# Kernel optimization log

Hardware: AMD Instinct MI355X
Metric: run time of the kernel (lower is better)

The kernel has to match this reference:

```python
import jax, jax.numpy as jnp
import numpy as np

NT_SIZES = {"paper": 100000, "author": 200000, "subject": 1000}
NT_FEATS = {"paper": 512, "author": 256, "subject": 128}
ET = [("paper", "author"), ("author", "paper"), ("paper", "subject"), ("subject", "paper")]
E_COUNTS = {("paper", "author"): 800000, ("author", "paper"): 800000,
            ("paper", "subject"): 100000, ("subject", "paper"): 100000}
HOP = 5
NHID = 64
NOUT = 16
# edge types sourced at each node type (order follows ET / edge_id mapping)
SRC_IDS = {"paper": [0, 2], "author": [1], "subject": [3]}


def setup_inputs() -> dict:
    key = jax.random.key(0)
    ks = iter(jax.random.split(key, 40))
    inp = {}
    # node features
    inp["x_paper"] = jax.random.normal(next(ks), (NT_SIZES["paper"], NT_FEATS["paper"]), jnp.float32)
    inp["x_author"] = jax.random.normal(next(ks), (NT_SIZES["author"], NT_FEATS["author"]), jnp.float32)
    inp["x_subject"] = jax.random.normal(next(ks), (NT_SIZES["subject"], NT_FEATS["subject"]), jnp.float32)
    # fc1 per node type (torch Linear layout: [out, in]), scaled ~1/sqrt(fan_in)
    for nt in NT_SIZES:
        fin = NT_FEATS[nt]
        inp[f"fc1_{nt}_w"] = jax.random.normal(next(ks), (NHID, fin), jnp.float32) / np.sqrt(fin)
        inp[f"fc1_{nt}_b"] = jnp.zeros((NHID,), jnp.float32)
    # attention vectors per hop per edge type; small scale keeps exp() stable
    inp["attn1_w"] = jax.random.normal(next(ks), (HOP, len(ET), NHID), jnp.float32) * 0.01
    inp["attn2_w"] = jax.random.normal(next(ks), (HOP, len(ET), NHID), jnp.float32) * 0.01
    inp["lw_w"] = jax.random.normal(next(ks), (HOP, len(ET)), jnp.float32)
    inp["fc2_w"] = jax.random.normal(next(ks), (NOUT, NHID), jnp.float32) / np.sqrt(NHID)
    inp["fc2_b"] = jnp.zeros((NOUT,), jnp.float32)
    # edge indices: row 0 = source (in src node-type range), row 1 = target
    for (s_nt, t_nt) in ET:
        E = E_COUNTS[(s_nt, t_nt)]
        s = jax.random.randint(next(ks), (E,), 0, NT_SIZES[s_nt], jnp.int32)
        t = jax.random.randint(next(ks), (E,), 0, NT_SIZES[t_nt], jnp.int32)
        inp[f"ei_{s_nt[0]}{t_nt[0]}"] = jnp.stack([s, t])
    return inp


def reference(x_paper, x_author, x_subject,
              fc1_paper_w, fc1_paper_b, fc1_author_w, fc1_author_b,
              fc1_subject_w, fc1_subject_b,
              attn1_w, attn2_w, lw_w, fc2_w, fc2_b,
              ei_pa, ei_ap, ei_ps, ei_sp):
    x_in = {"paper": x_paper, "author": x_author, "subject": x_subject}
    fc1 = {"paper": (fc1_paper_w, fc1_paper_b),
           "author": (fc1_author_w, fc1_author_b),
           "subject": (fc1_subject_w, fc1_subject_b)}
    edges = {ET[0]: ei_pa, ET[1]: ei_ap, ET[2]: ei_ps, ET[3]: ei_sp}

    # input projection (dropout = identity in eval mode)
    x_dict = {nt: jax.nn.relu(x_in[nt] @ fc1[nt][0].T + fc1[nt][1]) for nt in x_in}
    h_dict = dict(x_dict)

    for i in range(HOP):
        aggr = {nt: [] for nt in x_dict}
        for k, et in enumerate(ET):
            s_nt, t_nt = et
            ei = edges[et]
            s, t = ei[0], ei[1]
            x = x_dict[s_nt]            # [Ns, D]
            h = h_dict[t_nt]            # [Nt, D]
            N = x.shape[0]
            a1 = attn1_w[i, k]          # [D]
            a2 = attn2_w[i, k]          # [D]
            x1 = x @ a1                 # [Ns]
            h1 = h @ a2                 # [Nt]
            w2 = jnp.exp(jax.nn.leaky_relu(x1 + x @ a2, 0.2))            # [Ns] self term
            w1 = jnp.exp(jax.nn.leaky_relu(x1[s] + h1[t], 0.2))          # [E]  edge term
            div = jax.ops.segment_sum(w1, s, num_segments=N) + w2        # [Ns]
            num = jax.ops.segment_sum(w1[:, None] * h[t], s, num_segments=N) + w2[:, None] * x
            aggr[s_nt].append(num / div[:, None])
        for nt in x_dict:
            ids = jnp.array(SRC_IDS[nt])
            w = jax.nn.softmax(lw_w[i, ids])                             # learnable per-edge-type mix
            stacked = jnp.stack(aggr[nt], axis=1)                        # [N, K, D]
            h_dict[nt] = jax.nn.elu(jnp.einsum('nkd,k->nd', stacked, w))
    return h_dict["paper"] @ fc2_w.T + fc2_b
```

## Files before the change

kernel.cpp:

```cpp
#include <hip/hip_runtime.h>
#include <hip/hip_bf16.h>


#define NP 100000
#define NA 200000
#define NSJ 1000
#define EPA 800000
#define EAP 800000
#define EPS 100000
#define ESP 100000
#define ETOT 1800000
#define NS_TOT 401000
#define NT_TOT 401000
#define NSRC 301000
#define NCHUNK 392
#define NSGRP 25063
#define SCAT_SLICE 4096
#define NSLICE ((ETOT + SCAT_SLICE - 1) / SCAT_SLICE)
#define BKT ((ETOT + 7) / 8)

typedef __attribute__((ext_vector_type(8))) short bf16x8;
typedef __attribute__((ext_vector_type(4))) float floatx4;
typedef __attribute__((ext_vector_type(8))) float floatx8;
typedef __hip_bfloat16 bf16;

__device__ __forceinline__ float bf2f(bf16 v) { return __bfloat162float(v); }
__device__ __forceinline__ float us2f(unsigned short u) { return __uint_as_float((unsigned)u << 16); }
__device__ __forceinline__ float eluf(float x) { return x > 0.f ? x : __expf(x) - 1.f; }
__device__ __forceinline__ unsigned short f2bf_bits(float f) {
    unsigned int u = __float_as_uint(f);
    return (unsigned short)((u + 0x7FFFu + ((u >> 16) & 1u)) >> 16);
}

__device__ __forceinline__ bf16x8 load_frag_f32(const void* base, size_t off) {
    const float4* f = (const float4*)((const float*)base + off);
    float4 a = f[0], b = f[1];
    bf16x8 r;
    r[0] = (short)f2bf_bits(a.x); r[1] = (short)f2bf_bits(a.y);
    r[2] = (short)f2bf_bits(a.z); r[3] = (short)f2bf_bits(a.w);
    r[4] = (short)f2bf_bits(b.x); r[5] = (short)f2bf_bits(b.y);
    r[6] = (short)f2bf_bits(b.z); r[7] = (short)f2bf_bits(b.w);
    return r;
}

__device__ __forceinline__ int edge_src(int e, const int* pa, const int* ap,
                                        const int* ps, const int* sp) {
    if (e < EPA)                  return pa[e];
    if (e < EPA + EAP)            return NP + ap[e - EPA];
    if (e < EPA + EAP + EPS)      return NP + NA + ps[e - (EPA + EAP)];
    return NP + NA + NP + sp[e - (EPA + EAP + EPS)];
}
__device__ __forceinline__ int edge_tgt(int e, const int* pa, const int* ap,
                                        const int* ps, const int* sp) {
    if (e < EPA)                  return pa[EPA + e];
    if (e < EPA + EAP)            return ap[EAP + (e - EPA)];
    if (e < EPA + EAP + EPS)      return ps[EPS + (e - (EPA + EAP))];
    return sp[ESP + (e - (EPA + EAP + EPS))];
}

__global__ void detect_dtype(const unsigned int* __restrict__ xraw, int* __restrict__ flag) {
    int t = threadIdx.x;
    int hits = 0;
#pragma unroll
    for (int i = 0; i < 16; ++i) {
        unsigned int w = xraw[t * 16 + i];
        unsigned int lo = w & 0xFFFFu;
        unsigned int e = (lo >> 7) & 0xFFu;
        if (lo == 0u || (e >= 110u && e <= 140u)) hits++;
    }
#pragma unroll
    for (int o = 32; o; o >>= 1) hits += __shfl_xor(hits, o);
    if (t == 0) *flag = (hits > 512) ? 1 : 0;
}

__global__ void conv_all(const void* a1, const void* a2, const void* lw, const void* w2,
                         const void* b2, const void* bp, const void* ba, const void* bs,
                         float* a1c, float* a2c, float* lwc, float* w2c, float* b2c,
                         float* b1p, float* b1a, float* b1s, const int* __restrict__ flagp)
{
    int i = blockIdx.x * blockDim.x + threadIdx.x;
    int isb = *flagp;
    auto cv = [&](const void* s, int j) -> float {
        return isb ? bf2f(((const bf16*)s)[j]) : ((const float*)s)[j];
    };
    if (i < 1280)      a1c[i] = cv(a1, i);
    else if (i < 2560) a2c[i - 1280] = cv(a2, i - 1280);
    else if (i < 2580) lwc[i - 2560] = cv(lw, i - 2560);
    else if (i < 3604) w2c[i - 2580] = cv(w2, i - 2580);
    else if (i < 3620) b2c[i - 3604] = cv(b2, i - 3604);
    else if (i < 3684) b1p[i - 3620] = cv(bp, i - 3620);
    else if (i < 3748) b1a[i - 3684] = cv(ba, i - 3684);
    else if (i < 3812) b1s[i - 3748] = cv(bs, i - 3748);
}

__global__ void pack_attn(const float* __restrict__ a1c, const float* __restrict__ a2c,
                          bf16* __restrict__ apack)
{
    int i = blockIdx.x * blockDim.x + threadIdx.x;
    if (i >= 4096) return;
    int k = i >> 10, rf = i & 1023;
    int row = rf >> 6;
    int f = rf & 63;
    float v = 0.f;
    if (row < 5)       v = a1c[(row * 4 + k) * 64 + f];
    else if (row < 10) v = a2c[((row - 5) * 4 + k) * 64 + f];
    unsigned short hi = f2bf_bits(v);
    float lo = v - us2f(hi);
    unsigned short* up = (unsigned short*)apack;
    up[(size_t)(k * 2) * 1024 + rf]     = hi;
    up[(size_t)(k * 2 + 1) * 1024 + rf] = f2bf_bits(lo);
}

template<int K>
__global__ void fc1_t(const void* __restrict__ X, const void* __restrict__ W,
                      const float* __restrict__ B, int N,
                      bf16* __restrict__ xo, const int* __restrict__ flagp)
{
    constexpr int NK = K / 32;
    int isb = *flagp;
    int lane = threadIdx.x & 63;
    int wv = threadIdx.x >> 6;
    int grp = blockIdx.x * 4 + wv;
    int ngrp = (N + 15) >> 4;
    if (grp >= ngrp) return;
    int m = lane & 15, kq = lane >> 4;
    floatx4 acc[4] = {};
    int arow = grp * 16 + m;
    if (arow >= N) arow = N - 1;
    if (isb) {
        const bf16* Xb = (const bf16*)X + (size_t)arow * K + kq * 8;
        bf16x8 av[NK];
#pragma unroll
        for (int i = 0; i < NK; ++i) av[i] = *(const bf16x8*)(Xb + i * 32);
        const bf16* Wb = (const bf16*)W + (size_t)m * K + kq * 8;
#pragma unroll
        for (int i = 0; i < NK; ++i) {
#pragma unroll
            for (int nb = 0; nb < 4; ++nb) {
                bf16x8 bv = *(const bf16x8*)(Wb + (size_t)(nb * 16) * K + i * 32);
                acc[nb] = __builtin_amdgcn_mfma_f32_16x16x32_bf16(av[i], bv, acc[nb], 0, 0, 0);
            }
        }
    } else {
#pragma unroll 4
        for (int i = 0; i < NK; ++i) {
            int k0 = i * 32 + kq * 8;
            bf16x8 av = load_frag_f32(X, (size_t)arow * K + k0);
#pragma unroll
            for (int nb = 0; nb < 4; ++nb) {
                bf16x8 bv = load_frag_f32(W, (size_t)(nb * 16 + m) * K + k0);
                acc[nb] = __builtin_amdgcn_mfma_f32_16x16x32_bf16(av, bv, acc[nb], 0, 0, 0);
            }
        }
    }
#pragma unroll
    for (int nb = 0; nb < 4; ++nb) {
#pragma unroll
        for (int r = 0; r < 4; ++r) {
            int row = grp * 16 + kq * 4 + r;
            if (row < N) {
                int f = nb * 16 + m;
                float v = acc[nb][r] + B[f];
                xo[(size_t)row * 64 + f] = __float2bfloat16(fmaxf(v, 0.f));
            }
        }
    }
}

__global__ void precompute_xw_mfma(const bf16* __restrict__ xP, const bf16* __restrict__ xA,
                                   const bf16* __restrict__ xS,
                                   const bf16* __restrict__ apack,
                                   float* __restrict__ x1buf, float* __restrict__ w2buf)
{
    int wv = threadIdx.x >> 6;
    int lane = threadIdx.x & 63;
    int grp = blockIdx.x * 4 + wv;
    if (grp >= NSGRP) return;
    int base = grp * 16;
    int k, n0, nmax; const bf16* x;
    if (base < NP)                { k = 0; n0 = base;                  nmax = NP;  x = xP; }
    else if (base < NP + NA)      { k = 1; n0 = base - NP;             nmax = NA;  x = xA; }
    else if (base < NP + NA + NP) { k = 2; n0 = base - (NP + NA);      nmax = NP;  x = xP; }
    else                          { k = 3; n0 = base - (NP + NA + NP); nmax = NSJ; x = xS; }
    int m = lane & 15, kq = lane >> 4;
    int arow = n0 + m;
    if (arow >= nmax) arow = nmax - 1;
    const bf16* bh = apack + (size_t)(k * 2) * 1024;
    const bf16* bl = bh + 1024;
    floatx4 acc = {};
#pragma unroll
    for (int ks = 0; ks < 64; ks += 32) {
        int k0 = ks + kq * 8;
        bf16x8 av  = *(const bf16x8*)(x  + (size_t)arow * 64 + k0);
        bf16x8 bvh = *(const bf16x8*)(bh + m * 64 + k0);
        bf16x8 bvl = *(const bf16x8*)(bl + m * 64 + k0);
        acc = __builtin_amdgcn_mfma_f32_16x16x32_bf16(av, bvh, acc, 0, 0, 0);
        acc = __builtin_amdgcn_mfma_f32_16x16x32_bf16(av, bvl, acc, 0, 0, 0);
    }
#pragma unroll
    for (int r = 0; r < 4; ++r) {
        float v = acc[r];
        float d2 = __shfl(v, lane + 5);
        int node = base + kq * 4 + r;
        if (m < 5 && node < NS_TOT) {
            x1buf[m * NS_TOT + node] = v;
            float z = v + d2;
            w2buf[m * NS_TOT + node] = __expf(z > 0.f ? z : 0.2f * z);
        }
    }
}

__global__ void csr_rank(const int* __restrict__ pa, const int* __restrict__ ap,
                         const int* __restrict__ ps, const int* __restrict__ sp,
                         int* __restrict__ cnt, int* __restrict__ rank)
{
    int e = blockIdx.x * blockDim.x + threadIdx.x;
    if (e >= ETOT) return;
    int g = edge_src(e, pa, ap, ps, sp);
    rank[e] = atomicAdd(&cnt[g], 1);
}

__global__ void scan_reduce(const int* __restrict__ cnt, int* __restrict__ partial)
{
    __shared__ int s[256];
    int base = blockIdx.x * 1024 + threadIdx.x * 4;
    int sum = 0;
#pragma unroll
    for (int r = 0; r < 4; ++r) { int i = base + r; if (i < NS_TOT) sum += cnt[i]; }
    s[threadIdx.x] = sum; __syncthreads();
    for (int o = 128; o; o >>= 1) {
        if (threadIdx.x < o) s[threadIdx.x] += s[threadIdx.x + o];
        __syncthreads();
    }
    if (!threadIdx.x) partial[blockIdx.x] = s[0];
}

__global__ void scan_partials(const int* __restrict__ partial, int* __restrict__ chunkoff)
{
    __shared__ int s[512];
    int t = threadIdx.x;
    int v = (t < NCHUNK) ? partial[t] : 0;
    s[t] = v; __syncthreads();
    for (int o = 1; o < 512; o <<= 1) {
        int add = (t >= o) ? s[t - o] : 0;
        __syncthreads();
        s[t] += add; __syncthreads();
    }
    if (t < NCHUNK) chunkoff[t] = s[t] - v;
}

__global__ void scan_write(const int* __restrict__ cnt, const int* __restrict__ chunkoff,
                           int* __restrict__ off)
{
    __shared__ int s[256];
    int t = threadIdx.x;
    int base = blockIdx.x * 1024 + t * 4;
    int v[4]; int tsum = 0;
#pragma unroll
    for (int r = 0; r < 4; ++r) { int i = base + r; v[r] = (i < NS_TOT) ? cnt[i] : 0; tsum += v[r]; }
    s[t] = tsum; __syncthreads();
    for (int o = 1; o < 256; o <<= 1) {
        int add = (t >= o) ? s[t - o] : 0;
        __syncthreads();
        s[t] += add; __syncthreads();
    }
    int excl = s[t] - tsum + chunkoff[blockIdx.x];
#pragma unroll
    for (int r = 0; r < 4; ++r) {
        int i = base + r;
        if (i < NS_TOT) { off[i] = excl; excl += v[r]; }
    }
}

__global__ void csr_pos(const int* __restrict__ pa, const int* __restrict__ ap,
                        const int* __restrict__ ps, const int* __restrict__ sp,
                        const int* __restrict__ rank, const int* __restrict__ off,
                        int* __restrict__ pos)
{
    int e = blockIdx.x * blockDim.x + threadIdx.x;
    if (e >= ETOT) return;
    int g = edge_src(e, pa, ap, ps, sp);
    pos[e] = off[g] + rank[e];
}

__global__ void csr_scatter(const int* __restrict__ pa, const int* __restrict__ ap,
                            const int* __restrict__ ps, const int* __restrict__ sp,
                            const int* __restrict__ pos, int* __restrict__ col)
{
    int b = blockIdx.x & 7;
    int slice = blockIdx.x >> 3;
    int lo = b * BKT;
    int hi = lo + BKT; if (hi > ETOT) hi = ETOT;
    int ebase = slice * SCAT_SLICE;
    int eend = ebase + SCAT_SLICE; if (eend > ETOT) eend = ETOT;
    for (int e = ebase + threadIdx.x; e < eend; e += 256) {
        int p = pos[e];
        if (p < lo || p >= hi) continue;
        col[p] = edge_tgt(e, pa, ap, ps, sp);
    }
}

__global__ void hop_h1(const bf16* __restrict__ hP, const bf16* __restrict__ hA,
                       const bf16* __restrict__ hS,
                       const float* __restrict__ attn2, int hop, float* __restrict__ h1)
{
    int wave = (blockIdx.x * blockDim.x + threadIdx.x) >> 6;
    int lane = threadIdx.x & 63;
    int q = lane >> 4, fl = lane & 15;
    int wid = wave * 4 + q;
    if (wid >= NT_TOT) return;
    int k, n; const bf16* h;
    if (wid < NA)                 { k = 0; n = wid;               h = hA; }
    else if (wid < NA + NP)       { k = 1; n = wid - NA;          h = hP; }
    else if (wid < NA + NP + NSJ) { k = 2; n = wid - (NA + NP);   h = hS; }
    else                          { k = 3; n = wid - (NA+NP+NSJ); h = hP; }
    ushort4 hv = *(const ushort4*)((const unsigned short*)h + (size_t)n * 64 + fl * 4);
    const float4 a2 = *(const float4*)(attn2 + (hop * 4 + k) * 64 + fl * 4);
    float v = us2f(hv.x) * a2.x + us2f(hv.y) * a2.y + us2f(hv.z) * a2.z + us2f(hv.w) * a2.w;
#pragma unroll
    for (int o = 1; o <= 8; o <<= 1) v += __shfl_xor(v, o);
    if (fl == 0) h1[wid] = v;
}

__device__ __forceinline__ floatx8 agg_et8(int g, int hop, int eo, int fl, floatx8 xv,
    const float* __restrict__ x1buf, const float* __restrict__ w2buf,
    const float* __restrict__ h1, int h1base, const bf16* __restrict__ ht,
    const int* __restrict__ off, const int* __restrict__ deg, const int* __restrict__ col)
{
    float x1v = x1buf[hop * NS_TOT + g];
    floatx8 acc = {};
    float dv = 0.f;
    int e0 = off[g];
    int e1 = e0 + deg[g];
    for (int e = e0 + eo; e < e1; e += 8) {
        int t = col[e];
        float z = x1v + h1[h1base + t];
        float w1 = __expf(z > 0.f ? z : 0.2f * z);
        bf16x8 hv = *(const bf16x8*)(ht + (size_t)t * 64 + fl * 8);
#pragma unroll
        for (int j = 0; j < 8; ++j)
            acc[j] = fmaf(w1, us2f((unsigned short)hv[j]), acc[j]);
        dv += w1;
    }
#pragma unroll
    for (int o = 8; o <= 32; o <<= 1) {
#pragma unroll
        for (int j = 0; j < 8; ++j) acc[j] += __shfl_xor(acc[j], o);
        dv += __shfl_xor(dv, o);
    }
    float w2v = w2buf[hop * NS_TOT + g];
    dv += w2v;
    float inv = 1.f / dv;
    floatx8 r;
#pragma unroll
    for (int j = 0; j < 8; ++j) r[j] = (acc[j] + w2v * xv[j]) * inv;
    return r;
}

__global__ void hop_agg(const bf16* __restrict__ hPo, const bf16* __restrict__ hAo,
                        const bf16* __restrict__ hSo,
                        const bf16* __restrict__ xP, const bf16* __restrict__ xA,
                        const bf16* __restrict__ xS,
                        const float* __restrict__ x1buf, const float* __restrict__ w2buf,
                        const float* __restrict__ h1,
                        const int* __restrict__ off, const int* __restrict__ deg,
                        const int* __restrict__ col,
                        const float* __restrict__ lw, int hop,
                        bf16* __restrict__ hPn, bf16* __restrict__ hAn, bf16* __restrict__ hSn)
{
    int wid = (blockIdx.x * blockDim.x + threadIdx.x) >> 6;
    int lane = threadIdx.x & 63;
    int eo = lane >> 3, fl = lane & 7;
    if (wid >= NSRC) return;
    floatx8 r;
    bf16* dst;
    int n;
    if (wid < NP) {
        n = wid;
        bf16x8 xu = *(const bf16x8*)(xP + (size_t)n * 64 + fl * 8);
        floatx8 xv;
#pragma unroll
        for (int j = 0; j < 8; ++j) xv[j] = us2f((unsigned short)xu[j]);
        floatx8 r0 = agg_et8(n,           hop, eo, fl, xv, x1buf, w2buf, h1, 0,       hAo, off, deg, col);
        floatx8 r2 = agg_et8(NP + NA + n, hop, eo, fl, xv, x1buf, w2buf, h1, NA + NP, hSo, off, deg, col);
        float l0 = lw[hop * 4 + 0], l2 = lw[hop * 4 + 2];
        float mx = fmaxf(l0, l2);
        float e0 = __expf(l0 - mx), e2 = __expf(l2 - mx);
        float inv = 1.f / (e0 + e2);
#pragma unroll
        for (int j = 0; j < 8; ++j) r[j] = (e0 * r0[j] + e2 * r2[j]) * inv;
        dst = hPn;
    } else if (wid < NP + NA) {
        n = wid - NP;
        bf16x8 xu = *(const bf16x8*)(xA + (size_t)n * 64 + fl * 8);
        floatx8 xv;
#pragma unroll
        for (int j = 0; j < 8; ++j) xv[j] = us2f((unsigned short)xu[j]);
        r = agg_et8(NP + n, hop, eo, fl, xv, x1buf, w2buf, h1, NA, hPo, off, deg, col);
        dst = hAn;
    } else {
        n = wid - (NP + NA);
        bf16x8 xu = *(const bf16x8*)(xS + (size_t)n * 64 + fl * 8);
        floatx8 xv;
#pragma unroll
        for (int j = 0; j < 8; ++j) xv[j] = us2f((unsigned short)xu[j]);
        r = agg_et8(NP + NA + NP + n, hop, eo, fl, xv, x1buf, w2buf, h1, NA + NP + NSJ, hPo, off, deg, col);
        dst = hSn;
    }
    if (eo == 0) {
        bf16x8 st;
#pragma unroll
        for (int j = 0; j < 8; ++j) st[j] = (short)f2bf_bits(eluf(r[j]));
        *(bf16x8*)(dst + (size_t)n * 64 + fl * 8) = st;
    }
}

__global__ void fc2_kernel(const bf16* __restrict__ hP, const float* __restrict__ W2,
                           const float* __restrict__ B2, void* __restrict__ out,
                           const int* __restrict__ flagp)
{
    int isb = *flagp;
    int idx = blockIdx.x * blockDim.x + threadIdx.x;
    if (idx >= NP * 16) return;
    int n = idx >> 4, o = idx & 15;
    float acc = B2[o];
    const bf16* hr = hP + (size_t)n * 64;
#pragma unroll
    for (int j = 0; j < 64; ++j) acc = fmaf(bf2f(hr[j]), W2[o * 64 + j], acc);
    if (isb) ((bf16*)out)[idx] = __float2bfloat16(acc);
    else     ((float*)out)[idx] = acc;
}

extern "C" void kernel_launch(void* const* d_in, const int* in_sizes, int n_in,
                              void* d_out, int out_size, void* d_ws, size_t ws_size,
                              hipStream_t stream)
{
    (void)in_sizes; (void)n_in; (void)out_size; (void)ws_size;
    const void* xPi  = d_in[0];
    const void* xAi  = d_in[1];
    const void* xSi  = d_in[2];
    const void* f1pw = d_in[3];
    const void* f1pb = d_in[4];
    const void* f1aw = d_in[5];
    const void* f1ab = d_in[6];
    const void* f1sw = d_in[7];
    const void* f1sb = d_in[8];
    const void* attn1 = d_in[9];
    const void* attn2 = d_in[10];
    const void* lwp  = d_in[11];
    const void* f2w  = d_in[12];
    const void* f2b  = d_in[13];
    const int* eipa = (const int*)d_in[14];
    const int* eiap = (const int*)d_in[15];
    const int* eips = (const int*)d_in[16];
    const int* eisp = (const int*)d_in[17];

    char* p = (char*)d_ws;
    auto alloc = [&](size_t bytes) { char* r = p; p += (bytes + 255) & ~(size_t)255; return r; };
    int*  flag = (int*)alloc(4);
    bf16* xP = (bf16*)alloc((size_t)NP * 64 * 2);
    bf16* xA = (bf16*)alloc((size_t)NA * 64 * 2);
    bf16* xS = (bf16*)alloc((size_t)NSJ * 64 * 2);
    bf16* hb[2][3];
    for (int qq = 0; qq < 2; ++qq) {
        hb[qq][0] = (bf16*)alloc((size_t)NP * 64 * 2);
        hb[qq][1] = (bf16*)alloc((size_t)NA * 64 * 2);
        hb[qq][2] = (bf16*)alloc((size_t)NSJ * 64 * 2);
    }
    float* x1buf = (float*)alloc((size_t)5 * NS_TOT * 4);
    float* w2buf = (float*)alloc((size_t)5 * NS_TOT * 4);
    float* h1v  = (float*)alloc((size_t)NT_TOT * 4);
    int* cnt   = (int*)alloc((size_t)NS_TOT * 4);
    int* off   = (int*)alloc((size_t)NS_TOT * 4);
    int* rankv = (int*)alloc((size_t)ETOT * 4);
    int* posv  = (int*)alloc((size_t)ETOT * 4);
    int* colv  = (int*)alloc((size_t)ETOT * 4);
    int* partial  = (int*)alloc(512 * 4);
    int* chunkoff = (int*)alloc(512 * 4);
    float* a1c = (float*)alloc(1280 * 4);
    float* a2c = (float*)alloc(1280 * 4);
    float* lwc = (float*)alloc(20 * 4);
    float* w2c = (float*)alloc(1024 * 4);
    float* b2c = (float*)alloc(16 * 4);
    float* b1p = (float*)alloc(64 * 4);
    float* b1a = (float*)alloc(64 * 4);
    float* b1s = (float*)alloc(64 * 4);
    bf16* apack = (bf16*)alloc((size_t)4 * 2 * 1024 * 2);

    detect_dtype<<<1, 64, 0, stream>>>((const unsigned int*)xPi, flag);
    conv_all<<<15, 256, 0, stream>>>(attn1, attn2, lwp, f2w, f2b, f1pb, f1ab, f1sb,
                                     a1c, a2c, lwc, w2c, b2c, b1p, b1a, b1s, flag);
    pack_attn<<<16, 256, 0, stream>>>(a1c, a2c, apack);

    fc1_t<512><<<(6250 + 3) / 4, 256, 0, stream>>>(xPi, f1pw, b1p, NP, xP, flag);
    fc1_t<256><<<(12500 + 3) / 4, 256, 0, stream>>>(xAi, f1aw, b1a, NA, xA, flag);
    fc1_t<128><<<(63 + 3) / 4, 256, 0, stream>>>(xSi, f1sw, b1s, NSJ, xS, flag);

    precompute_xw_mfma<<<(NSGRP + 3) / 4, 256, 0, stream>>>(xP, xA, xS, apack, x1buf, w2buf);

    hipMemsetAsync(cnt, 0, (size_t)NS_TOT * 4, stream);
    csr_rank<<<(ETOT + 255) / 256, 256, 0, stream>>>(eipa, eiap, eips, eisp, cnt, rankv);
    scan_reduce<<<NCHUNK, 256, 0, stream>>>(cnt, partial);
    scan_partials<<<1, 512, 0, stream>>>(partial, chunkoff);
    scan_write<<<NCHUNK, 256, 0, stream>>>(cnt, chunkoff, off);
    csr_pos<<<(ETOT + 255) / 256, 256, 0, stream>>>(eipa, eiap, eips, eisp, rankv, off, posv);
    csr_scatter<<<NSLICE * 8, 256, 0, stream>>>(eipa, eiap, eips, eisp, posv, colv);

    const bf16* cP = xP; const bf16* cA = xA; const bf16* cS = xS;
    for (int i = 0; i < 5; ++i) {
        bf16* nPb = hb[i & 1][0]; bf16* nAb = hb[i & 1][1]; bf16* nSb = hb[i & 1][2];
        hop_h1<<<(NT_TOT + 15) / 16, 256, 0, stream>>>(cP, cA, cS, a2c, i, h1v);
        hop_agg<<<(NSRC + 3) / 4, 256, 0, stream>>>(cP, cA, cS, xP, xA, xS,
                                                    x1buf, w2buf, h1v, off, cnt, colv,
                                                    lwc, i, nPb, nAb, nSb);
        cP = nPb; cA = nAb; cS = nSb;
    }

    fc2_kernel<<<(NP * 16 + 255) / 256, 256, 0, stream>>>(cP, w2c, b2c, d_out, flag);
}
```

Baseline: 1.606 ms.

## Fuse target attention dot into edge aggregation and stage fc1 inputs through LDS

Removes the separate per-hop h1 kernel and computes the target-side attention dot product inside the aggregation loop, reusing the already loaded target feature vector and reducing across the 8 lanes with shuffles. This drops one launch and one extra gather of h1 per edge, at the cost of redundant dot-product work per edge instead of once per node. Separately, the bf16 fc1 path now stages input rows into double-buffered, XOR-swizzled LDS using direct global-to-LDS loads, with 64 rows per block. That path only runs when the inputs are bf16, which may not be the default.

```diff
diff --git a/kernel.cpp b/kernel.cpp
--- a/kernel.cpp
+++ b/kernel.cpp
@@ -11,7 +11,6 @@
 #define ESP 100000
 #define ETOT 1800000
 #define NS_TOT 401000
-#define NT_TOT 401000
 #define NSRC 301000
 #define NCHUNK 392
 #define NSGRP 25063
@@ -30,6 +29,12 @@
 __device__ __forceinline__ unsigned short f2bf_bits(float f) {
     unsigned int u = __float_as_uint(f);
     return (unsigned short)((u + 0x7FFFu + ((u >> 16) & 1u)) >> 16);
+}
+
+__device__ __forceinline__ void gload_lds16(const void* g, void* l) {
+    __builtin_amdgcn_global_load_lds(
+        (const __attribute__((address_space(1))) unsigned int*)g,
+        (__attribute__((address_space(3))) unsigned int*)l, 16, 0, 0);
 }
 
 __device__ __forceinline__ bf16x8 load_frag_f32(const void* base, size_t off) {
@@ -112,38 +117,62 @@
 }
 
 template<int K>
-__global__ void fc1_t(const void* __restrict__ X, const void* __restrict__ W,
-                      const float* __restrict__ B, int N,
-                      bf16* __restrict__ xo, const int* __restrict__ flagp)
-{
-    constexpr int NK = K / 32;
+__global__ void fc1_lds(const void* __restrict__ X, const void* __restrict__ W,
+                        const float* __restrict__ Bb, int N,
+                        bf16* __restrict__ xo, const int* __restrict__ flagp)
+{
+    constexpr int NSTEP = K / 128;
+    __shared__ __align__(16) unsigned char lds[2][64 * 256];
     int isb = *flagp;
     int lane = threadIdx.x & 63;
     int wv = threadIdx.x >> 6;
-    int grp = blockIdx.x * 4 + wv;
-    int ngrp = (N + 15) >> 4;
-    if (grp >= ngrp) return;
+    int row0 = blockIdx.x * 64;
     int m = lane & 15, kq = lane >> 4;
     floatx4 acc[4] = {};
-    int arow = grp * 16 + m;
-    if (arow >= N) arow = N - 1;
+
     if (isb) {
-        const bf16* Xb = (const bf16*)X + (size_t)arow * K + kq * 8;
-        bf16x8 av[NK];
-#pragma unroll
-        for (int i = 0; i < NK; ++i) av[i] = *(const bf16x8*)(Xb + i * 32);
-        const bf16* Wb = (const bf16*)W + (size_t)m * K + kq * 8;
-#pragma unroll
-        for (int i = 0; i < NK; ++i) {
-#pragma unroll
-            for (int nb = 0; nb < 4; ++nb) {
-                bf16x8 bv = *(const bf16x8*)(Wb + (size_t)(nb * 16) * K + i * 32);
-                acc[nb] = __builtin_amdgcn_mfma_f32_16x16x32_bf16(av[i], bv, acc[nb], 0, 0, 0);
+        const bf16* Xb = (const bf16*)X;
+        const bf16* Wb = (const bf16*)W;
+        auto stage = [&](int s, int b) {
+#pragma unroll
+            for (int it = 0; it < 4; ++it) {
+                int slotbase = (it * 4 + wv) * 64;
+                int slot = slotbase + lane;
+                int r = slot >> 4;
+                int c = slot & 15;
+                int rc = row0 + r; if (rc >= N) rc = N - 1;
+                int cs = c ^ (r & 15);
+                const bf16* src = Xb + (size_t)rc * K + s * 128 + cs * 8;
+                gload_lds16(src, &lds[b][slotbase * 16]);
             }
+        };
+        stage(0, 0);
+        asm volatile("s_waitcnt vmcnt(0)" ::: "memory");
+        __syncthreads();
+        int R = wv * 16 + m;
+#pragma unroll
+        for (int s = 0; s < NSTEP; ++s) {
+            if (s + 1 < NSTEP) stage(s + 1, (s + 1) & 1);
+            const unsigned char* bufp = lds[s & 1];
+#pragma unroll
+            for (int i = 0; i < 4; ++i) {
+                int cs = (i * 4 + kq) ^ (R & 15);
+                bf16x8 av = *(const bf16x8*)(bufp + R * 256 + cs * 16);
+                int kg = s * 128 + i * 32 + kq * 8;
+#pragma unroll
+                for (int nb = 0; nb < 4; ++nb) {
+                    bf16x8 bv = *(const bf16x8*)(Wb + (size_t)(nb * 16 + m) * K + kg);
+                    acc[nb] = __builtin_amdgcn_mfma_f32_16x16x32_bf16(av, bv, acc[nb], 0, 0, 0);
+                }
+            }
+            asm volatile("s_waitcnt vmcnt(0)" ::: "memory");
+            __syncthreads();
         }
     } else {
+        int arow = row0 + wv * 16 + m;
+        if (arow >= N) arow = N - 1;
 #pragma unroll 4
-        for (int i = 0; i < NK; ++i) {
+        for (int i = 0; i < K / 32; ++i) {
             int k0 = i * 32 + kq * 8;
             bf16x8 av = load_frag_f32(X, (size_t)arow * K + k0);
 #pragma unroll
@@ -157,10 +186,10 @@
     for (int nb = 0; nb < 4; ++nb) {
 #pragma unroll
         for (int r = 0; r < 4; ++r) {
-            int row = grp * 16 + kq * 4 + r;
+            int row = row0 + wv * 16 + kq * 4 + r;
             if (row < N) {
                 int f = nb * 16 + m;
-                float v = acc[nb][r] + B[f];
+                float v = acc[nb][r] + Bb[f];
                 xo[(size_t)row * 64 + f] = __float2bfloat16(fmaxf(v, 0.f));
             }
         }
@@ -300,46 +329,36 @@
     }
 }
 
-__global__ void hop_h1(const bf16* __restrict__ hP, const bf16* __restrict__ hA,
-                       const bf16* __restrict__ hS,
-                       const float* __restrict__ attn2, int hop, float* __restrict__ h1)
-{
-    int wave = (blockIdx.x * blockDim.x + threadIdx.x) >> 6;
-    int lane = threadIdx.x & 63;
-    int q = lane >> 4, fl = lane & 15;
-    int wid = wave * 4 + q;
-    if (wid >= NT_TOT) return;
-    int k, n; const bf16* h;
-    if (wid < NA)                 { k = 0; n = wid;               h = hA; }
-    else if (wid < NA + NP)       { k = 1; n = wid - NA;          h = hP; }
-    else if (wid < NA + NP + NSJ) { k = 2; n = wid - (NA + NP);   h = hS; }
-    else                          { k = 3; n = wid - (NA+NP+NSJ); h = hP; }
-    ushort4 hv = *(const ushort4*)((const unsigned short*)h + (size_t)n * 64 + fl * 4);
-    const float4 a2 = *(const float4*)(attn2 + (hop * 4 + k) * 64 + fl * 4);
-    float v = us2f(hv.x) * a2.x + us2f(hv.y) * a2.y + us2f(hv.z) * a2.z + us2f(hv.w) * a2.w;
-#pragma unroll
-    for (int o = 1; o <= 8; o <<= 1) v += __shfl_xor(v, o);
-    if (fl == 0) h1[wid] = v;
-}
-
-__device__ __forceinline__ floatx8 agg_et8(int g, int hop, int eo, int fl, floatx8 xv,
+__device__ __forceinline__ floatx8 agg_et8(int g, int hop, int k, int eo, int fl, floatx8 xv,
     const float* __restrict__ x1buf, const float* __restrict__ w2buf,
-    const float* __restrict__ h1, int h1base, const bf16* __restrict__ ht,
+    const float* __restrict__ a2c, const bf16* __restrict__ ht,
     const int* __restrict__ off, const int* __restrict__ deg, const int* __restrict__ col)
 {
     float x1v = x1buf[hop * NS_TOT + g];
+    const float4* a2p = (const float4*)(a2c + (hop * 4 + k) * 64 + fl * 8);
+    float4 a2a = a2p[0], a2b = a2p[1];
     floatx8 acc = {};
     float dv = 0.f;
     int e0 = off[g];
     int e1 = e0 + deg[g];
     for (int e = e0 + eo; e < e1; e += 8) {
         int t = col[e];
-        float z = x1v + h1[h1base + t];
+        bf16x8 hv = *(const bf16x8*)(ht + (size_t)t * 64 + fl * 8);
+        float hf[8];
+#pragma unroll
+        for (int j = 0; j < 8; ++j) hf[j] = us2f((unsigned short)hv[j]);
+        float h1t = hf[0] * a2a.x;
+        h1t = fmaf(hf[1], a2a.y, h1t); h1t = fmaf(hf[2], a2a.z, h1t);
+        h1t = fmaf(hf[3], a2a.w, h1t); h1t = fmaf(hf[4], a2b.x, h1t);
+        h1t = fmaf(hf[5], a2b.y, h1t); h1t = fmaf(hf[6], a2b.z, h1t);
+        h1t = fmaf(hf[7], a2b.w, h1t);
+        h1t += __shfl_xor(h1t, 1);
+        h1t += __shfl_xor(h1t, 2);
+        h1t += __shfl_xor(h1t, 4);
+        float z = x1v + h1t;
         float w1 = __expf(z > 0.f ? z : 0.2f * z);
-        bf16x8 hv = *(const bf16x8*)(ht + (size_t)t * 64 + fl * 8);
-#pragma unroll
-        for (int j = 0; j < 8; ++j)
-            acc[j] = fmaf(w1, us2f((unsigned short)hv[j]), acc[j]);
+#pragma unroll
+        for (int j = 0; j < 8; ++j) acc[j] = fmaf(w1, hf[j], acc[j]);
         dv += w1;
     }
 #pragma unroll
@@ -362,7 +381,7 @@
                         const bf16* __restrict__ xP, const bf16* __restrict__ xA,
                         const bf16* __restrict__ xS,
                         const float* __restrict__ x1buf, const float* __restrict__ w2buf,
-                        const float* __restrict__ h1,
+                        const float* __restrict__ a2c,
                         const int* __restrict__ off, const int* __restrict__ deg,
                         const int* __restrict__ col,
                         const float* __restrict__ lw, int hop,
@@ -381,8 +400,8 @@
         floatx8 xv;
 #pragma unroll
         for (int j = 0; j < 8; ++j) xv[j] = us2f((unsigned short)xu[j]);
-        floatx8 r0 = agg_et8(n,           hop, eo, fl, xv, x1buf, w2buf, h1, 0,       hAo, off, deg, col);
-        floatx8 r2 = agg_et8(NP + NA + n, hop, eo, fl, xv, x1buf, w2buf, h1, NA + NP, hSo, off, deg, col);
+        floatx8 r0 = agg_et8(n,           hop, 0, eo, fl, xv, x1buf, w2buf, a2c, hAo, off, deg, col);
+        floatx8 r2 = agg_et8(NP + NA + n, hop, 2, eo, fl, xv, x1buf, w2buf, a2c, hSo, off, deg, col);
         float l0 = lw[hop * 4 + 0], l2 = lw[hop * 4 + 2];
         float mx = fmaxf(l0, l2);
         float e0 = __expf(l0 - mx), e2 = __expf(l2 - mx);
@@ -396,7 +415,7 @@
         floatx8 xv;
 #pragma unroll
         for (int j = 0; j < 8; ++j) xv[j] = us2f((unsigned short)xu[j]);
-        r = agg_et8(NP + n, hop, eo, fl, xv, x1buf, w2buf, h1, NA, hPo, off, deg, col);
+        r = agg_et8(NP + n, hop, 1, eo, fl, xv, x1buf, w2buf, a2c, hPo, off, deg, col);
         dst = hAn;
     } else {
         n = wid - (NP + NA);
@@ -404,7 +423,7 @@
         floatx8 xv;
 #pragma unroll
         for (int j = 0; j < 8; ++j) xv[j] = us2f((unsigned short)xu[j]);
-        r = agg_et8(NP + NA + NP + n, hop, eo, fl, xv, x1buf, w2buf, h1, NA + NP + NSJ, hPo, off, deg, col);
+        r = agg_et8(NP + NA + NP + n, hop, 3, eo, fl, xv, x1buf, w2buf, a2c, hPo, off, deg, col);
         dst = hSn;
     }
     if (eo == 0) {
@@ -469,7 +488,6 @@
     }
     float* x1buf = (float*)alloc((size_t)5 * NS_TOT * 4);
     float* w2buf = (float*)alloc((size_t)5 * NS_TOT * 4);
-    float* h1v  = (float*)alloc((size_t)NT_TOT * 4);
     int* cnt   = (int*)alloc((size_t)NS_TOT * 4);
     int* off   = (int*)alloc((size_t)NS_TOT * 4);
     int* rankv = (int*)alloc((size_t)ETOT * 4);
@@ -492,9 +510,9 @@
                                      a1c, a2c, lwc, w2c, b2c, b1p, b1a, b1s, flag);
     pack_attn<<<16, 256, 0, stream>>>(a1c, a2c, apack);
 
-    fc1_t<512><<<(6250 + 3) / 4, 256, 0, stream>>>(xPi, f1pw, b1p, NP, xP, flag);
-    fc1_t<256><<<(12500 + 3) / 4, 256, 0, stream>>>(xAi, f1aw, b1a, NA, xA, flag);
-    fc1_t<128><<<(63 + 3) / 4, 256, 0, stream>>>(xSi, f1sw, b1s, NSJ, xS, flag);
+    fc1_lds<512><<<(NP + 63) / 64, 256, 0, stream>>>(xPi, f1pw, b1p, NP, xP, flag);
+    fc1_lds<256><<<(NA + 63) / 64, 256, 0, stream>>>(xAi, f1aw, b1a, NA, xA, flag);
+    fc1_lds<128><<<(NSJ + 63) / 64, 256, 0, stream>>>(xSi, f1sw, b1s, NSJ, xS, flag);
 
     precompute_xw_mfma<<<(NSGRP + 3) / 4, 256, 0, stream>>>(xP, xA, xS, apack, x1buf, w2buf);
 
@@ -509,9 +527,8 @@
     const bf16* cP = xP; const bf16* cA = xA; const bf16* cS = xS;
     for (int i = 0; i < 5; ++i) {
         bf16* nPb = hb[i & 1][0]; bf16* nAb = hb[i & 1][1]; bf16* nSb = hb[i & 1][2];
-        hop_h1<<<(NT_TOT + 15) / 16, 256, 0, stream>>>(cP, cA, cS, a2c, i, h1v);
         hop_agg<<<(NSRC + 3) / 4, 256, 0, stream>>>(cP, cA, cS, xP, xA, xS,
-                                                    x1buf, w2buf, h1v, off, cnt, colv,
+                                                    x1buf, w2buf, a2c, off, cnt, colv,
                                                     lwc, i, nPb, nAb, nSb);
         cP = nPb; cA = nAb; cS = nSb;
     }
```

After: 1.657 ms. 3.2% more time.
